# Performance work log

Hardware: AMD Instinct MI355X
Metric: run time of the kernel (lower is better)

Reference implementation:

```python
import jax, jax.numpy as jnp
import numpy as np

E = 1024   # embed_dim
H = 1024   # hidden_dim
NH = 16    # num_heads
HD = H // NH
B, P, C = 2, 1024, 1024


def _layernorm(x, g, b):
    m = jnp.mean(x, axis=-1, keepdims=True)
    v = jnp.mean((x - m) ** 2, axis=-1, keepdims=True)
    return (x - m) / jnp.sqrt(v + 1e-5) * g + b


def _attention(problem, context, Wq, bq, Wk, bk, Wv, bv, mask, num_heads, head_dim, head_out_dim):
    # Faithful to source: head axis LAST in the reshape, mask added AFTER softmax.
    batch = problem.shape[0]
    q = (problem @ Wq + bq).reshape(batch, -1, head_dim, num_heads)      # b i d h
    k = (context @ Wk + bk).reshape(batch, -1, head_dim, num_heads)      # b j d h
    v = (context @ Wv + bv).reshape(batch, -1, head_out_dim, num_heads)  # b j o h
    scores = jnp.einsum('bidh,bjdh->bijh', q, k) / jnp.sqrt(jnp.asarray(head_dim, q.dtype))
    p = jax.nn.softmax(scores, axis=2)
    if mask is not None:
        p = p + mask[..., None]
    out = jnp.einsum('bijh,bjoh->bioh', p, v)
    return out.reshape(batch, -1, head_out_dim * num_heads)


def setup_inputs() -> dict:
    key = jax.random.key(0)
    ks = jax.random.split(key, 20)
    s = 0.02
    inp = {
        'x': jax.random.normal(ks[0], (B, P, E), jnp.float32),
        'context': jax.random.normal(ks[1], (B, C, E), jnp.float32),
        'causal_mask': jnp.zeros((B, P, P), jnp.float32),
        'problem_pad_mask': jnp.zeros((B, P, P), jnp.float32),
        'context_pad_mask': jnp.zeros((B, P, C), jnp.float32),
        # self-attn params (out_dim = E)
        'sa_Wq': jax.random.normal(ks[2], (E, H), jnp.float32) * s, 'sa_bq': jnp.zeros((H,), jnp.float32),
        'sa_Wk': jax.random.normal(ks[3], (E, H), jnp.float32) * s, 'sa_bk': jnp.zeros((H,), jnp.float32),
        'sa_Wv': jax.random.normal(ks[4], (E, E), jnp.float32) * s, 'sa_bv': jnp.zeros((E,), jnp.float32),
        # cross-attn params
        'ca_Wq': jax.random.normal(ks[5], (E, H), jnp.float32) * s, 'ca_bq': jnp.zeros((H,), jnp.float32),
        'ca_Wk': jax.random.normal(ks[6], (E, H), jnp.float32) * s, 'ca_bk': jnp.zeros((H,), jnp.float32),
        'ca_Wv': jax.random.normal(ks[7], (E, E), jnp.float32) * s, 'ca_bv': jnp.zeros((E,), jnp.float32),
        # layernorms
        'ln1_g': jnp.ones((E,), jnp.float32), 'ln1_b': jnp.zeros((E,), jnp.float32),
        'ln2_g': jnp.ones((E,), jnp.float32), 'ln2_b': jnp.zeros((E,), jnp.float32),
        'ln3_g': jnp.ones((E,), jnp.float32), 'ln3_b': jnp.zeros((E,), jnp.float32),
        # mlp
        'mlp_W1': jax.random.normal(ks[8], (E, H), jnp.float32) * s, 'mlp_b1': jnp.zeros((H,), jnp.float32),
        'mlp_W2': jax.random.normal(ks[9], (H, E), jnp.float32) * s, 'mlp_b2': jnp.zeros((E,), jnp.float32),
    }
    return inp


def reference(x, context, causal_mask, problem_pad_mask, context_pad_mask,
              sa_Wq, sa_bq, sa_Wk, sa_bk, sa_Wv, sa_bv,
              ca_Wq, ca_bq, ca_Wk, ca_bk, ca_Wv, ca_bv,
              ln1_g, ln1_b, ln2_g, ln2_b, ln3_g, ln3_b,
              mlp_W1, mlp_b1, mlp_W2, mlp_b2):
    self_attn_mask = causal_mask + problem_pad_mask
    xc = x
    x = _attention(x, x, sa_Wq, sa_bq, sa_Wk, sa_bk, sa_Wv, sa_bv, self_attn_mask, NH, HD, E // NH)
    x = _layernorm(x, ln1_g, ln1_b) + xc
    xc = x
    x = _attention(x, context, ca_Wq, ca_bq, ca_Wk, ca_bk, ca_Wv, ca_bv, context_pad_mask, NH, HD, E // NH)
    x = _layernorm(x, ln2_g, ln2_b) + xc
    xc = x
    x = jax.nn.relu(x @ mlp_W1 + mlp_b1) @ mlp_W2 + mlp_b2
    return _layernorm(x, ln3_g, ln3_b) + xc
```

## Files before the change

### kernel.cpp

```cpp
#include <hip/hip_runtime.h>
#include <math.h>

#define NHEADS 16

typedef __attribute__((ext_vector_type(8))) short bf16x8;
typedef __attribute__((ext_vector_type(4))) float f32x4;

__device__ inline short f2b(float f) {
  unsigned u = __float_as_uint(f);
  u += 0x7fffu + ((u >> 16) & 1u);
  return (short)(u >> 16);
}
__device__ inline float b2f(short s) {
  return __uint_as_float(((unsigned)(unsigned short)s) << 16);
}
__device__ inline void gld16(const void* g, void* l) {
  __builtin_amdgcn_global_load_lds(
      (const __attribute__((address_space(1))) unsigned int*)g,
      (__attribute__((address_space(3))) unsigned int*)l, 16, 0, 0);
}
#define MFMA16(a, b, c) __builtin_amdgcn_mfma_f32_16x16x32_bf16(a, b, c, 0, 0, 0)

__global__ __launch_bounds__(256) void prep_wt(
    const float* __restrict__ x, const float* __restrict__ ctx,
    const float* __restrict__ cm, const float* __restrict__ ppm,
    const float* __restrict__ cpm,
    const float* sabq, const float* sabk, const float* sabv,
    const float* cabk, const float* cabv, const float* cabq,
    const float* W0, const float* W1, const float* W2, const float* W3,
    const float* W4, const float* W5, const float* W6, const float* W7,
    short* __restrict__ XB, short* __restrict__ CTXB,
    short* __restrict__ MBSA, short* __restrict__ MBCA,
    float* __restrict__ qkvb, float* __restrict__ kvb,
    float* __restrict__ qpb, unsigned* __restrict__ kmaxu,
    short* __restrict__ WT) {
  __shared__ float t[64][65];
  const int blk = blockIdx.x;
  const int tid = threadIdx.x;
  const int n4 = 2048 * 1024 / 4;
  if (blk < 8192) {
    int seg = blk >> 11;
    int i = (blk & 2047) * 256 + tid;
    if (i >= n4) return;
    float4 va;
    short* out;
    if (seg == 0) { va = ((const float4*)x)[i]; out = XB; }
    else if (seg == 1) { va = ((const float4*)ctx)[i]; out = CTXB; }
    else if (seg == 2) {
      va = ((const float4*)cm)[i];
      float4 vb = ((const float4*)ppm)[i];
      va.x += vb.x; va.y += vb.y; va.z += vb.z; va.w += vb.w;
      out = MBSA;
    } else { va = ((const float4*)cpm)[i]; out = MBCA; }
    short4 s;
    s.x = f2b(va.x); s.y = f2b(va.y); s.z = f2b(va.z); s.w = f2b(va.w);
    ((short4*)out)[i] = s;
    return;
  }
  if (blk < 8216) {
    if (blk == 8192 && tid < 64) kmaxu[tid] = 0u;
    int i = (blk - 8192) * 256 + tid;
    if (i >= 6144) return;
    int j = i & 1023;
    int pj = ((j & 63) << 4) | (j >> 6);
    int sec = i >> 10;
    if (sec == 0) qkvb[j] = sabq[pj];
    else if (sec == 1) qkvb[1024 + j] = sabk[pj];
    else if (sec == 2) qkvb[2048 + j] = sabv[pj];
    else if (sec == 3) kvb[j] = cabk[pj];
    else if (sec == 4) kvb[1024 + j] = cabv[pj];
    else qpb[j] = cabq[pj];
    return;
  }
  const int blk2 = blk - 8216;
  const int wz = blk2 >> 8;
  const int rem = blk2 & 255;
  const float* W;
  switch (wz) {
    case 0: W = W0; break; case 1: W = W1; break;
    case 2: W = W2; break; case 3: W = W3; break;
    case 4: W = W4; break; case 5: W = W5; break;
    case 6: W = W6; break; default: W = W7; break;
  }
  const int permute = (wz < 6) ? 1 : 0;
  short* o = WT + (size_t)wz * 1024 * 1024;
  const int n0 = (rem & 15) * 64, k0 = (rem >> 4) * 64;
  const int cg = (tid & 15) * 4, rg = tid >> 4;
  #pragma unroll
  for (int r = 0; r < 4; ++r) {
    int kl = rg + r * 16;
    float4 v = *(const float4*)(W + (size_t)(k0 + kl) * 1024 + n0 + cg);
    t[kl][cg + 0] = v.x; t[kl][cg + 1] = v.y;
    t[kl][cg + 2] = v.z; t[kl][cg + 3] = v.w;
  }
  __syncthreads();
  #pragma unroll
  for (int r = 0; r < 4; ++r) {
    int nl = rg + r * 16;
    int n = n0 + nl;
    int nrow = permute ? (((n & 15) << 6) | (n >> 4)) : n;
    short4 s;
    s.x = f2b(t[cg + 0][nl]); s.y = f2b(t[cg + 1][nl]);
    s.z = f2b(t[cg + 2][nl]); s.w = f2b(t[cg + 3][nl]);
    *(short4*)(o + (size_t)nrow * 1024 + k0 + cg) = s;
  }
}

template <int TN>
__global__ __launch_bounds__(256) void gemmT(
    const short* __restrict__ A, const short* __restrict__ Bt,
    const float* __restrict__ bias,
    void* __restrict__ C0, short* __restrict__ C1, short* __restrict__ C2,
    int mode, int relu, int ny,
    const short* __restrict__ A2, const short* __restrict__ Bt2,
    const float* __restrict__ bias2,
    void* __restrict__ D0, short* __restrict__ D1, short* __restrict__ D2,
    int mode2, int relu2, int ny2,
    unsigned* __restrict__ kout) {
  if (blockIdx.z == 1) {
    A = A2; Bt = Bt2; bias = bias2;
    C0 = D0; C1 = D1; C2 = D2; mode = mode2; relu = relu2; ny = ny2;
  }
  if ((int)blockIdx.y >= ny) return;

  constexpr int NT = TN / 32;
  constexpr int BR = TN / 4;
  __shared__ short As[64 * 64];
  __shared__ short Bs[TN * 64];
  const int tid = threadIdx.x;
  const int w = tid >> 6, l = tid & 63;
  const int ln = l & 15, lq = l >> 4;
  const int wm = w >> 1, wn = w & 1;
  const int m0 = blockIdx.x * 64, n0 = blockIdx.y * TN;
  const int K = 1024;

  f32x4 acc[2][NT];
  #pragma unroll
  for (int s = 0; s < 2; ++s)
    #pragma unroll
    for (int t = 0; t < NT; ++t) acc[s][t] = (f32x4){0.f, 0.f, 0.f, 0.f};

  const int srow = l >> 3;
  const int sch = (l & 7) ^ srow;
  const short* ga = A + (size_t)(m0 + w * 16 + srow) * K + sch * 8;
  const short* gb = Bt + (size_t)(n0 + w * BR + srow) * K + sch * 8;
  short* la = &As[w * 16 * 64];
  short* lb = &Bs[w * BR * 64];

  for (int k0 = 0; k0 < K; k0 += 64) {
    __syncthreads();
    gld16(ga + k0, la);
    gld16(ga + (size_t)8 * K + k0, la + 512);
    #pragma unroll
    for (int rb = 0; rb < BR / 8; ++rb)
      gld16(gb + (size_t)rb * 8 * K + k0, lb + rb * 512);
    __syncthreads();
    #pragma unroll
    for (int kc = 0; kc < 2; ++kc) {
      const int co = ((kc * 4 + lq) ^ (ln & 7)) * 8;
      bf16x8 af[2], bf[NT];
      af[0] = *(const bf16x8*)&As[(wm * 32 + ln) * 64 + co];
      af[1] = *(const bf16x8*)&As[(wm * 32 + 16 + ln) * 64 + co];
      #pragma unroll
      for (int t = 0; t < NT; ++t)
        bf[t] = *(const bf16x8*)&Bs[(wn * (TN / 2) + t * 16 + ln) * 64 + co];
      #pragma unroll
      for (int s = 0; s < 2; ++s)
        #pragma unroll
        for (int t = 0; t < NT; ++t)
          acc[s][t] = MFMA16(af[s], bf[t], acc[s][t]);
    }
  }

  float bv[NT];
  #pragma unroll
  for (int t = 0; t < NT; ++t) bv[t] = bias[n0 + wn * (TN / 2) + t * 16 + ln];

  #pragma unroll
  for (int s = 0; s < 2; ++s) {
    #pragma unroll
    for (int t = 0; t < NT; ++t) {
      #pragma unroll
      for (int r = 0; r < 4; ++r) {
        int m = m0 + wm * 32 + s * 16 + lq * 4 + r;
        int n = n0 + wn * (TN / 2) + t * 16 + ln;
        float v = acc[s][t][r] + bv[t];
        if (relu) v = fmaxf(v, 0.f);
        int bb = m >> 10, ii = m & 1023;
        if (mode == 0) {
          ((float*)C0)[(size_t)m * 1024 + n] = v;
        } else if (mode == 1) {
          ((short*)C0)[(size_t)m * 1024 + n] = f2b(v);
        } else if (mode == 2) {
          int hh = n >> 6, d = n & 63;
          ((short*)C0)[(((size_t)(bb * 16 + hh)) * 1024 + ii) * 64 + d] = f2b(v);
        } else if (mode == 3) {
          int sel = n >> 10, g = n & 1023;
          int hh = g >> 6, d = g & 63;
          if (sel == 0)
            ((short*)C0)[(((size_t)(bb * 16 + hh)) * 1024 + ii) * 64 + d] = f2b(v);
          else if (sel == 1)
            C1[(((size_t)(bb * 16 + hh)) * 1024 + ii) * 64 + d] = f2b(v);
          else
            C2[(((size_t)(bb * 16 + hh)) * 64 + d) * 1024 + ii] = f2b(v);
        } else {
          int sel = n >> 10, g = n & 1023;
          int hh = g >> 6, d = g & 63;
          if (sel == 0)
            C1[(((size_t)(bb * 16 + hh)) * 1024 + ii) * 64 + d] = f2b(v);
          else
            C2[(((size_t)(bb * 16 + hh)) * 64 + d) * 1024 + ii] = f2b(v);
        }
      }
    }
  }

  if constexpr (TN == 128) {
    const int nb = n0 + wn * 64;
    const int selw = nb >> 10;
    if ((mode == 3 && selw == 1) || (mode == 4 && selw == 0)) {
      const int slotbase = (mode == 3) ? 0 : 32;
      const int bb = m0 >> 10;
      const int hh = (nb & 1023) >> 6;
      float mx = 0.f;
      #pragma unroll
      for (int s = 0; s < 2; ++s)
        #pragma unroll
        for (int r = 0; r < 4; ++r) {
          float ss = 0.f;
          #pragma unroll
          for (int t = 0; t < 4; ++t) {
            float v = acc[s][t][r] + bv[t];
            ss += v * v;
          }
          ss += __shfl_xor(ss, 1, 64);
          ss += __shfl_xor(ss, 2, 64);
          ss += __shfl_xor(ss, 4, 64);
          ss += __shfl_xor(ss, 8, 64);
          mx = fmaxf(mx, ss);
        }
      mx = fmaxf(mx, __shfl_xor(mx, 16, 64));
      mx = fmaxf(mx, __shfl_xor(mx, 32, 64));
      if (l == 0)
        atomicMax(kout + slotbase + bb * 16 + hh, __float_as_uint(mx));
    }
  }
}

__global__ __launch_bounds__(256) void attn_flash(
    const short* __restrict__ qh, const short* __restrict__ kh,
    const short* __restrict__ vt, const short* __restrict__ maskb,
    const unsigned* __restrict__ kmax, float* __restrict__ out) {
  __shared__ short Ks[128 * 64];
  __shared__ short Vs[64 * 128];
  __shared__ short Msk[64 * 128];
  __shared__ short Ps[4][16 * 72];
  __shared__ float Ml[64];
  const int tid = threadIdx.x;
  const int w = tid >> 6, l = tid & 63;
  const int ln = l & 15, lq = l >> 4;
  const int i0 = blockIdx.x * 64;
  const int b = blockIdx.z;
  const int bh = b * 16 + blockIdx.y;
  const size_t bho = (size_t)bh * 65536;

  const short* qp = qh + bho + (size_t)(i0 + w * 16 + ln) * 64 + lq * 8;
  bf16x8 qf0 = *(const bf16x8*)qp;
  bf16x8 qf1 = *(const bf16x8*)(qp + 32);

  float ssq = 0.f;
  #pragma unroll
  for (int e = 0; e < 8; ++e) {
    float f0 = b2f(qf0[e]), f1 = b2f(qf1[e]);
    ssq += f0 * f0 + f1 * f1;
  }
  ssq += __shfl_xor(ssq, 16, 64);
  ssq += __shfl_xor(ssq, 32, 64);
  float km = sqrtf(__uint_as_float(kmax[bh])) * 1.005f;
  if (lq == 0) Ml[w * 16 + ln] = sqrtf(ssq) * km * 0.125f + 1e-3f;
  float Mr[4], lac[4];
  #pragma unroll
  for (int r = 0; r < 4; ++r) { Mr[r] = Ml[w * 16 + lq * 4 + r]; lac[r] = 0.f; }

  const int r8 = l >> 3;
  const int c8 = (l & 7) ^ r8;
  const int r4 = l >> 4;
  const int cva = (l & 15) ^ r4;
  const short* gkb = kh + bho + (size_t)(w * 32 + r8) * 64 + c8 * 8;
  const short* gvb = vt + bho + (size_t)(w * 16 + r4) * 1024;
  const short* gmb = maskb + ((size_t)(b * 1024 + i0 + w * 16 + r4)) * 1024;
  short* lkb = &Ks[w * 32 * 64];
  short* lvb = &Vs[w * 16 * 128];
  short* lmb = &Msk[w * 16 * 128];
  short* PsW = &Ps[w][0];

  f32x4 oa[4], mo[4];
  #pragma unroll
  for (int os = 0; os < 4; ++os) {
    oa[os] = (f32x4){0.f, 0.f, 0.f, 0.f};
    mo[os] = (f32x4){0.f, 0.f, 0.f, 0.f};
  }

  const int c0 = (lq ^ (ln & 7)) * 8;
  const int c1 = ((4 | lq) ^ (ln & 7)) * 8;

  for (int jt = 0; jt < 8; ++jt) {
    const int j0 = jt * 128;
    __syncthreads();
    #pragma unroll
    for (int gi = 0; gi < 4; ++gi)
      gld16(gkb + (size_t)(j0 + gi * 8) * 64, lkb + gi * 512);
    #pragma unroll
    for (int gi = 0; gi < 4; ++gi) {
      int cc = (cva ^ ((gi & 1) << 2)) * 8;
      gld16(gvb + (size_t)gi * 4096 + j0 + cc, lvb + gi * 512);
      gld16(gmb + (size_t)gi * 4096 + j0 + cc, lmb + gi * 512);
    }
    __syncthreads();

    #pragma unroll
    for (int jh = 0; jh < 2; ++jh) {
      f32x4 sa[4];
      #pragma unroll
      for (int js = 0; js < 4; ++js) {
        const short* kr = &Ks[(jh * 64 + js * 16 + ln) * 64];
        bf16x8 kb0 = *(const bf16x8*)(kr + c0);
        bf16x8 kb1 = *(const bf16x8*)(kr + c1);
        f32x4 s = (f32x4){0.f, 0.f, 0.f, 0.f};
        s = MFMA16(qf0, kb0, s);
        s = MFMA16(qf1, kb1, s);
        sa[js] = s;
      }
      #pragma unroll
      for (int js = 0; js < 4; ++js)
        #pragma unroll
        for (int r = 0; r < 4; ++r) {
          float p = __expf(sa[js][r] * 0.125f - Mr[r]);
          lac[r] += p;
          PsW[(lq * 4 + r) * 72 + js * 16 + ln] = f2b(p);
        }
      bf16x8 pa0 = *(const bf16x8*)&PsW[ln * 72 + lq * 8];
      bf16x8 pa1 = *(const bf16x8*)&PsW[ln * 72 + 32 + lq * 8];
      const short* mr2 = &Msk[(w * 16 + ln) * 128 + jh * 64];
      bf16x8 ma0 = *(const bf16x8*)(mr2 + c0);
      bf16x8 ma1 = *(const bf16x8*)(mr2 + c1);
      #pragma unroll
      for (int os = 0; os < 4; ++os) {
        const short* vr = &Vs[(os * 16 + ln) * 128 + jh * 64];
        bf16x8 vb0 = *(const bf16x8*)(vr + c0);
        bf16x8 vb1 = *(const bf16x8*)(vr + c1);
        oa[os] = MFMA16(pa0, vb0, oa[os]);
        oa[os] = MFMA16(pa1, vb1, oa[os]);
        mo[os] = MFMA16(ma0, vb0, mo[os]);
        mo[os] = MFMA16(ma1, vb1, mo[os]);
      }
    }
  }

  #pragma unroll
  for (int r = 0; r < 4; ++r) {
    lac[r] += __shfl_xor(lac[r], 1, 64);
    lac[r] += __shfl_xor(lac[r], 2, 64);
    lac[r] += __shfl_xor(lac[r], 4, 64);
    lac[r] += __shfl_xor(lac[r], 8, 64);
  }
  float inv[4];
  #pragma unroll
  for (int r = 0; r < 4; ++r) inv[r] = 1.f / lac[r];

  #pragma unroll
  for (int os = 0; os < 4; ++os)
    #pragma unroll
    for (int r = 0; r < 4; ++r) {
      int row = i0 + w * 16 + lq * 4 + r;
      int o = os * 16 + ln;
      out[bho + (size_t)row * 64 + o] = oa[os][r] * inv[r] + mo[os][r];
    }
}

__global__ __launch_bounds__(256) void ln_kernel(
    const float* __restrict__ x, const short* __restrict__ res,
    const float* __restrict__ g, const float* __restrict__ be,
    void* __restrict__ outp, int out_bf16, int inmode) {
  const int row = blockIdx.x;
  const int tid = threadIdx.x;
  float4 v;
  if (inmode == 0) {
    v = ((const float4*)(x + (size_t)row * 1024))[tid];
  } else {
    int b = row >> 10, i = row & 1023;
    const float* base = x + (size_t)b * 16 * 65536 + (size_t)i * 64;
    int o = tid >> 2, h0 = (tid & 3) * 4;
    v.x = base[(size_t)(h0 + 0) * 65536 + o];
    v.y = base[(size_t)(h0 + 1) * 65536 + o];
    v.z = base[(size_t)(h0 + 2) * 65536 + o];
    v.w = base[(size_t)(h0 + 3) * 65536 + o];
  }
  float s = v.x + v.y + v.z + v.w;
  float sq = v.x * v.x + v.y * v.y + v.z * v.z + v.w * v.w;
  #pragma unroll
  for (int off = 32; off > 0; off >>= 1) {
    s += __shfl_down(s, off, 64);
    sq += __shfl_down(sq, off, 64);
  }
  __shared__ float rs[4], rq[4], stat[2];
  int wave = tid >> 6, lane = tid & 63;
  if (lane == 0) { rs[wave] = s; rq[wave] = sq; }
  __syncthreads();
  if (tid == 0) {
    float S = rs[0] + rs[1] + rs[2] + rs[3];
    float Q = rq[0] + rq[1] + rq[2] + rq[3];
    float mean = S * (1.f / 1024.f);
    float var = Q * (1.f / 1024.f) - mean * mean;
    stat[0] = mean;
    stat[1] = rsqrtf(var + 1e-5f);
  }
  __syncthreads();
  float mean = stat[0], rstd = stat[1];
  float4 g4 = ((const float4*)g)[tid];
  float4 b4 = ((const float4*)be)[tid];
  short4 r4 = ((const short4*)(res + (size_t)row * 1024))[tid];
  float o0 = (v.x - mean) * rstd * g4.x + b4.x + b2f(r4.x);
  float o1 = (v.y - mean) * rstd * g4.y + b4.y + b2f(r4.y);
  float o2 = (v.z - mean) * rstd * g4.z + b4.z + b2f(r4.z);
  float o3 = (v.w - mean) * rstd * g4.w + b4.w + b2f(r4.w);
  if (out_bf16) {
    short4 o;
    o.x = f2b(o0); o.y = f2b(o1); o.z = f2b(o2); o.w = f2b(o3);
    ((short4*)outp)[(size_t)row * 256 + tid] = o;
  } else {
    float4 o = {o0, o1, o2, o3};
    ((float4*)outp)[(size_t)row * 256 + tid] = o;
  }
}

extern "C" void kernel_launch(void* const* d_in, const int* in_sizes, int n_in,
                              void* d_out, int out_size, void* d_ws, size_t ws_size,
                              hipStream_t stream) {
  const float* x    = (const float*)d_in[0];
  const float* ctx  = (const float*)d_in[1];
  const float* cm   = (const float*)d_in[2];
  const float* ppm  = (const float*)d_in[3];
  const float* cpm  = (const float*)d_in[4];
  const float* saWq = (const float*)d_in[5];
  const float* sabq = (const float*)d_in[6];
  const float* saWk = (const float*)d_in[7];
  const float* sabk = (const float*)d_in[8];
  const float* saWv = (const float*)d_in[9];
  const float* sabv = (const float*)d_in[10];
  const float* caWq = (const float*)d_in[11];
  const float* cabq = (const float*)d_in[12];
  const float* caWk = (const float*)d_in[13];
  const float* cabk = (const float*)d_in[14];
  const float* caWv = (const float*)d_in[15];
  const float* cabv = (const float*)d_in[16];
  const float* ln1g = (const float*)d_in[17];
  const float* ln1b = (const float*)d_in[18];
  const float* ln2g = (const float*)d_in[19];
  const float* ln2b = (const float*)d_in[20];
  const float* ln3g = (const float*)d_in[21];
  const float* ln3b = (const float*)d_in[22];
  const float* W1   = (const float*)d_in[23];
  const float* b1   = (const float*)d_in[24];
  const float* W2   = (const float*)d_in[25];
  const float* b2   = (const float*)d_in[26];

  char* ws = (char*)d_ws;
  const size_t MB = 1024 * 1024;
  short* WT       = (short*)(ws);
  float* qkvb     = (float*)(ws + 16 * MB);
  float* kvb      = (float*)(ws + 16 * MB + 16384);
  float* qpb      = (float*)(ws + 16 * MB + 32768);
  unsigned* kmaxu = (unsigned*)(ws + 16 * MB + 49152);
  short* MBSA  = (short*)(ws + 17 * MB);
  short* MBCA  = (short*)(ws + 21 * MB);
  short* XB    = (short*)(ws + 25 * MB);
  short* CTXB  = (short*)(ws + 29 * MB);
  short* QH    = (short*)(ws + 33 * MB);
  short* KH    = (short*)(ws + 37 * MB);
  short* VT    = (short*)(ws + 41 * MB);
  float* S3    = (float*)(ws + 45 * MB);
  short* X1B   = (short*)(ws + 53 * MB);
  short* KH2   = (short*)(ws + 57 * MB);
  short* VT2   = (short*)(ws + 61 * MB);
  short* X2B   = MBSA;
  short* HB    = CTXB;
  float* outp  = (float*)d_out;

  dim3 lg(2048);
  const short* dsp = nullptr;
  const float* dfp = nullptr;

  prep_wt<<<dim3(10264), 256, 0, stream>>>(
      x, ctx, cm, ppm, cpm, sabq, sabk, sabv, cabk, cabv, cabq,
      saWq, saWk, saWv, caWk, caWv, caWq, W1, W2,
      XB, CTXB, MBSA, MBCA, qkvb, kvb, qpb, kmaxu, WT);

  gemmT<128><<<dim3(32, 24, 2), 256, 0, stream>>>(
      XB, WT, qkvb, QH, KH, VT, 3, 0, 24,
      CTXB, WT + 3 * 1048576, kvb, nullptr, KH2, VT2, 4, 0, 16, kmaxu);

  attn_flash<<<dim3(16, 16, 2), 256, 0, stream>>>(QH, KH, VT, MBSA, kmaxu, S3);
  ln_kernel<<<lg, 256, 0, stream>>>(S3, XB, ln1g, ln1b, X1B, 1, 1);

  gemmT<64><<<dim3(32, 16, 1), 256, 0, stream>>>(
      X1B, WT + 5 * 1048576, qpb, QH, nullptr, nullptr, 2, 0, 16,
      dsp, dsp, dfp, nullptr, nullptr, nullptr, 0, 0, 0, kmaxu);

  attn_flash<<<dim3(16, 16, 2), 256, 0, stream>>>(QH, KH2, VT2, MBCA,
                                                  kmaxu + 32, S3);
  ln_kernel<<<lg, 256, 0, stream>>>(S3, X1B, ln2g, ln2b, X2B, 1, 1);

  gemmT<64><<<dim3(32, 16, 1), 256, 0, stream>>>(
      X2B, WT + 6 * 1048576, b1, HB, nullptr, nullptr, 1, 1, 16,
      dsp, dsp, dfp, nullptr, nullptr, nullptr, 0, 0, 0, kmaxu);
  gemmT<64><<<dim3(32, 16, 1), 256, 0, stream>>>(
      HB, WT + 7 * 1048576, b2, S3, nullptr, nullptr, 0, 0, 16,
      dsp, dsp, dfp, nullptr, nullptr, nullptr, 0, 0, 0, kmaxu);
  ln_kernel<<<lg, 256, 0, stream>>>(S3, X2B, ln3g, ln3b, outp, 0, 0);
}
```

Baseline: 309.7 us.

## Store attention and MLP outputs in bf16 and regroup the projection GEMM launches

Attention outputs and the second MLP GEMM output are now written as bf16 instead of fp32. The layernorm kernel reads bf16 through a new input mode, which halves the intermediate traffic. The cross-attention K/V projection moves out of the first fused GEMM and into the cross-attention Q GEMM launch, which now uses 128-wide tiles, so the separate KH2/VT2 buffers go away. The cost is extra rounding of intermediates to bf16 before layernorm and residual.

After: 297.5 us. 3.9% less time.

```diff
diff --git a/kernel.cpp b/kernel.cpp
--- a/kernel.cpp
+++ b/kernel.cpp
@@ -250,7 +250,7 @@
 __global__ __launch_bounds__(256) void attn_flash(
     const short* __restrict__ qh, const short* __restrict__ kh,
     const short* __restrict__ vt, const short* __restrict__ maskb,
-    const unsigned* __restrict__ kmax, float* __restrict__ out) {
+    const unsigned* __restrict__ kmax, short* __restrict__ out) {
   __shared__ short Ks[128 * 64];
   __shared__ short Vs[64 * 128];
   __shared__ short Msk[64 * 128];
@@ -374,27 +374,31 @@
     for (int r = 0; r < 4; ++r) {
       int row = i0 + w * 16 + lq * 4 + r;
       int o = os * 16 + ln;
-      out[bho + (size_t)row * 64 + o] = oa[os][r] * inv[r] + mo[os][r];
+      out[bho + (size_t)row * 64 + o] = f2b(oa[os][r] * inv[r] + mo[os][r]);
     }
 }
 
 __global__ __launch_bounds__(256) void ln_kernel(
-    const float* __restrict__ x, const short* __restrict__ res,
+    const void* __restrict__ xin, const short* __restrict__ res,
     const float* __restrict__ g, const float* __restrict__ be,
     void* __restrict__ outp, int out_bf16, int inmode) {
   const int row = blockIdx.x;
   const int tid = threadIdx.x;
   float4 v;
   if (inmode == 0) {
-    v = ((const float4*)(x + (size_t)row * 1024))[tid];
+    v = ((const float4*)((const float*)xin + (size_t)row * 1024))[tid];
+  } else if (inmode == 1) {
+    int b = row >> 10, i = row & 1023;
+    const short* base = (const short*)xin + (size_t)b * 16 * 65536 +
+                        (size_t)i * 64;
+    int o = tid >> 2, h0 = (tid & 3) * 4;
+    v.x = b2f(base[(size_t)(h0 + 0) * 65536 + o]);
+    v.y = b2f(base[(size_t)(h0 + 1) * 65536 + o]);
+    v.z = b2f(base[(size_t)(h0 + 2) * 65536 + o]);
+    v.w = b2f(base[(size_t)(h0 + 3) * 65536 + o]);
   } else {
-    int b = row >> 10, i = row & 1023;
-    const float* base = x + (size_t)b * 16 * 65536 + (size_t)i * 64;
-    int o = tid >> 2, h0 = (tid & 3) * 4;
-    v.x = base[(size_t)(h0 + 0) * 65536 + o];
-    v.y = base[(size_t)(h0 + 1) * 65536 + o];
-    v.z = base[(size_t)(h0 + 2) * 65536 + o];
-    v.w = base[(size_t)(h0 + 3) * 65536 + o];
+    short4 s4 = ((const short4*)((const short*)xin + (size_t)row * 1024))[tid];
+    v.x = b2f(s4.x); v.y = b2f(s4.y); v.z = b2f(s4.z); v.w = b2f(s4.w);
   }
   float s = v.x + v.y + v.z + v.w;
   float sq = v.x * v.x + v.y * v.y + v.z * v.z + v.w * v.w;
@@ -479,10 +483,8 @@
   short* QH    = (short*)(ws + 33 * MB);
   short* KH    = (short*)(ws + 37 * MB);
   short* VT    = (short*)(ws + 41 * MB);
-  float* S3    = (float*)(ws + 45 * MB);
+  short* S3B   = (short*)(ws + 45 * MB);
   short* X1B   = (short*)(ws + 53 * MB);
-  short* KH2   = (short*)(ws + 57 * MB);
-  short* VT2   = (short*)(ws + 61 * MB);
   short* X2B   = MBSA;
   short* HB    = CTXB;
   float* outp  = (float*)d_out;
@@ -496,26 +498,26 @@
       saWq, saWk, saWv, caWk, caWv, caWq, W1, W2,
       XB, CTXB, MBSA, MBCA, qkvb, kvb, qpb, kmaxu, WT);
 
-  gemmT<128><<<dim3(32, 24, 2), 256, 0, stream>>>(
+  gemmT<128><<<dim3(32, 24, 1), 256, 0, stream>>>(
       XB, WT, qkvb, QH, KH, VT, 3, 0, 24,
-      CTXB, WT + 3 * 1048576, kvb, nullptr, KH2, VT2, 4, 0, 16, kmaxu);
-
-  attn_flash<<<dim3(16, 16, 2), 256, 0, stream>>>(QH, KH, VT, MBSA, kmaxu, S3);
-  ln_kernel<<<lg, 256, 0, stream>>>(S3, XB, ln1g, ln1b, X1B, 1, 1);
-
-  gemmT<64><<<dim3(32, 16, 1), 256, 0, stream>>>(
-      X1B, WT + 5 * 1048576, qpb, QH, nullptr, nullptr, 2, 0, 16,
       dsp, dsp, dfp, nullptr, nullptr, nullptr, 0, 0, 0, kmaxu);
 
-  attn_flash<<<dim3(16, 16, 2), 256, 0, stream>>>(QH, KH2, VT2, MBCA,
-                                                  kmaxu + 32, S3);
-  ln_kernel<<<lg, 256, 0, stream>>>(S3, X1B, ln2g, ln2b, X2B, 1, 1);
+  attn_flash<<<dim3(16, 16, 2), 256, 0, stream>>>(QH, KH, VT, MBSA, kmaxu, S3B);
+  ln_kernel<<<lg, 256, 0, stream>>>(S3B, XB, ln1g, ln1b, X1B, 1, 1);
+
+  gemmT<128><<<dim3(32, 16, 2), 256, 0, stream>>>(
+      X1B, WT + 5 * 1048576, qpb, QH, nullptr, nullptr, 2, 0, 8,
+      CTXB, WT + 3 * 1048576, kvb, nullptr, KH, VT, 4, 0, 16, kmaxu);
+
+  attn_flash<<<dim3(16, 16, 2), 256, 0, stream>>>(QH, KH, VT, MBCA,
+                                                  kmaxu + 32, S3B);
+  ln_kernel<<<lg, 256, 0, stream>>>(S3B, X1B, ln2g, ln2b, X2B, 1, 1);
 
   gemmT<64><<<dim3(32, 16, 1), 256, 0, stream>>>(
       X2B, WT + 6 * 1048576, b1, HB, nullptr, nullptr, 1, 1, 16,
       dsp, dsp, dfp, nullptr, nullptr, nullptr, 0, 0, 0, kmaxu);
   gemmT<64><<<dim3(32, 16, 1), 256, 0, stream>>>(
-      HB, WT + 7 * 1048576, b2, S3, nullptr, nullptr, 0, 0, 16,
+      HB, WT + 7 * 1048576, b2, S3B, nullptr, nullptr, 1, 0, 16,
       dsp, dsp, dfp, nullptr, nullptr, nullptr, 0, 0, 0, kmaxu);
-  ln_kernel<<<lg, 256, 0, stream>>>(S3, X2B, ln3g, ln3b, outp, 0, 0);
-}
+  ln_kernel<<<lg, 256, 0, stream>>>(S3B, X2B, ln3g, ln3b, outp, 0, 2);
+}
```
